# Performance work log

Measured on AMD Instinct MI355X. Metric: run time of the kernel, lower is better.

Reference implementation:

```python
import jax, jax.numpy as jnp
import numpy as np


def xenet_batch(x, a, e, sw, sb, aiw, aib, ajw, ajb, nw, nb, ew, eb):
    """Spektral XENetConvBatch: x (B,N,F), a (B,N,N), e (B,N,N,S)."""
    B, N, F = x.shape
    x_i = jnp.broadcast_to(x[:, :, None, :], (B, N, N, F))   # target node i per pair
    x_j = jnp.broadcast_to(x[:, None, :, :], (B, N, N, F))   # source node j per pair
    e_t = jnp.transpose(e, (0, 2, 1, 3))                      # reversed edge features
    stack = jnp.concatenate([x_i, x_j, e, e_t], axis=-1)      # (B,N,N,2F+2S)
    stack = jax.nn.relu(stack @ sw + sb)                      # stack MLP, (B,N,N,32)
    stack = stack * a[..., None]                              # mask/weight by adjacency
    att_i = jax.nn.sigmoid(stack @ aiw + aib)                 # incoming gate
    att_j = jax.nn.sigmoid(stack @ ajw + ajb)                 # outgoing gate
    agg_i = jnp.sum(att_i * stack, axis=2)                    # aggregate over sources j -> (B,N,32)
    agg_j = jnp.sum(att_j * stack, axis=1)                    # aggregate over targets i -> (B,N,32)
    x_out = jnp.concatenate([x, agg_i, agg_j], axis=-1) @ nw + nb  # node model (linear)
    e_out = stack @ ew + eb                                   # edge model (linear)
    return x_out, e_out


def setup_inputs() -> dict:
    key = jax.random.key(0)
    ks = jax.random.split(key, 16)
    B, N, F, S, C, L = 1, 400, 240, 1, 32, 1440
    SIN = 2 * F + 2 * S   # 482
    NIN = F + 2 * C       # 304
    s = 0.05
    inp = {
        "x": jax.random.normal(ks[0], (B, N, F), jnp.float32),
        "a": jax.random.uniform(ks[1], (B, N, N), jnp.float32),
        "e": jax.random.normal(ks[2], (B, N, N, S), jnp.float32),
        "c1_sw": jax.random.normal(ks[3], (SIN, C), jnp.float32) * s,
        "c1_sb": jnp.zeros((C,), jnp.float32),
        "c1_aiw": jax.random.normal(ks[4], (C, 1), jnp.float32) * s,
        "c1_aib": jnp.zeros((1,), jnp.float32),
        "c1_ajw": jax.random.normal(ks[5], (C, 1), jnp.float32) * s,
        "c1_ajb": jnp.zeros((1,), jnp.float32),
        "c1_nw": jax.random.normal(ks[6], (NIN, F), jnp.float32) * s,
        "c1_nb": jnp.zeros((F,), jnp.float32),
        "c1_ew": jax.random.normal(ks[7], (C, S), jnp.float32) * s,
        "c1_eb": jnp.zeros((S,), jnp.float32),
        "c2_sw": jax.random.normal(ks[8], (SIN, C), jnp.float32) * s,
        "c2_sb": jnp.zeros((C,), jnp.float32),
        "c2_aiw": jax.random.normal(ks[9], (C, 1), jnp.float32) * s,
        "c2_aib": jnp.zeros((1,), jnp.float32),
        "c2_ajw": jax.random.normal(ks[10], (C, 1), jnp.float32) * s,
        "c2_ajb": jnp.zeros((1,), jnp.float32),
        "c2_nw": jax.random.normal(ks[11], (NIN, F), jnp.float32) * s,
        "c2_nb": jnp.zeros((F,), jnp.float32),
        "c2_ew": jax.random.normal(ks[12], (C, S), jnp.float32) * s,
        "c2_eb": jnp.zeros((S,), jnp.float32),
        "dw": jax.random.normal(ks[13], (F, L), jnp.float32) * s,
        "db": jnp.zeros((L,), jnp.float32),
    }
    return inp


def reference(x, a, e,
              c1_sw, c1_sb, c1_aiw, c1_aib, c1_ajw, c1_ajb, c1_nw, c1_nb, c1_ew, c1_eb,
              c2_sw, c2_sb, c2_aiw, c2_aib, c2_ajw, c2_ajb, c2_nw, c2_nb, c2_ew, c2_eb,
              dw, db):
    x, e = xenet_batch(x, a, e, c1_sw, c1_sb, c1_aiw, c1_aib, c1_ajw, c1_ajb,
                       c1_nw, c1_nb, c1_ew, c1_eb)
    x, e = xenet_batch(x, a, e, c2_sw, c2_sb, c2_aiw, c2_aib, c2_ajw, c2_ajb,
                       c2_nw, c2_nb, c2_ew, c2_eb)
    return x @ dw + db  # (B, N, n_labels)
```

## Files before the change

kernel.cpp:

```cpp
#include <hip/hip_runtime.h>

#define NN 400
#define FF 240
#define CC 32
#define NIN 304
#define LL 1440

__global__ __launch_bounds__(256) void pq_kernel(
    const float* __restrict__ x, const float* __restrict__ sw,
    const float* __restrict__ sb, float* __restrict__ P, float* __restrict__ Q) {
    const int i0  = blockIdx.x * 4;
    const int t   = threadIdx.x;
    const int c   = t & 31;
    const int isQ = (t >> 5) & 1;
    const int g   = t >> 6;
    const float* wb = sw + (isQ ? FF * CC : 0) + c;
    const float bias = (!isQ && g == 0) ? sb[c] : 0.0f;
    float acc0 = bias, acc1 = bias, acc2 = bias, acc3 = bias;
    const float* xr = x + i0 * FF;
    const int f0 = g * 60;
    #pragma unroll 4
    for (int f = f0; f < f0 + 60; ++f) {
        const float w = wb[f * CC];
        acc0 += xr[f] * w;
        acc1 += xr[FF + f] * w;
        acc2 += xr[2 * FF + f] * w;
        acc3 += xr[3 * FF + f] * w;
    }
    __shared__ float red[4][256];
    const int slot = t & 63;
    red[g][slot]       = acc0;
    red[g][64 + slot]  = acc1;
    red[g][128 + slot] = acc2;
    red[g][192 + slot] = acc3;
    __syncthreads();
    {
        const int row = t >> 6, s2 = t & 63;
        const float s = red[0][row * 64 + s2] + red[1][row * 64 + s2]
                      + red[2][row * 64 + s2] + red[3][row * 64 + s2];
        const int i = i0 + row;
        if (s2 >= 32) Q[i * CC + (s2 & 31)] = s;
        else          P[i * CC + s2] = s;
    }
}

template<bool WRITE_E, bool DO_PQ>
__global__ __launch_bounds__(1024) void rcf_node(
    const float* __restrict__ P, const float* __restrict__ Q,
    const float* __restrict__ e, const float* __restrict__ a,
    const float* __restrict__ sw_tail,
    const float* __restrict__ aiw, const float* __restrict__ aib,
    const float* __restrict__ ajw, const float* __restrict__ ajb,
    const float* __restrict__ ew, const float* __restrict__ eb,
    float* __restrict__ e_out,
    const float* __restrict__ xin, const float* __restrict__ nw,
    const float* __restrict__ nb,
    const float* __restrict__ sw2, const float* __restrict__ sb2,
    float* __restrict__ xout, float* __restrict__ Pout, float* __restrict__ Qout) {
    const int bid  = blockIdx.x;
    const int base = (bid & 7) * 50 + (bid >> 3) * 2;
    const int t  = threadIdx.x;
    const int pg = t >> 3, l = t & 7, c0 = l * 4;

    __shared__ float smem[10816];
    float* red  = smem;
    float* vA   = smem + 9216;
    float* vB   = smem + 9520;
    float* xsA  = smem + 9824;
    float* xsB  = smem + 10064;
    float* part = smem + 10304;
    float* redn = smem;
    float* red2 = smem;

    if (t < FF) {
        vA[t] = xin[base * FF + t];
        vB[t] = xin[(base + 1) * FF + t];
    }

    float2 er2[4], ak2[4];
    int kk[4];
    #pragma unroll
    for (int it = 0; it < 4; ++it) {
        const int off = it * 128 + pg;
        kk[it] = (off < NN) ? off : 0;
        er2[it] = *(const float2*)(e + kk[it] * NN + base);
        ak2[it] = *(const float2*)(a + kk[it] * NN + base);
    }

    float w1v[4], w2v[4], wiv[4], wjv[4], wev[4];
    *(float4*)w1v = *(const float4*)(sw_tail + c0);
    *(float4*)w2v = *(const float4*)(sw_tail + CC + c0);
    *(float4*)wiv = *(const float4*)(aiw + c0);
    *(float4*)wjv = *(const float4*)(ajw + c0);
    if (WRITE_E) *(float4*)wev = *(const float4*)(ew + c0);
    const float bi = aib[0], bj = ajb[0];
    const float be = WRITE_E ? eb[0] : 0.0f;

    #pragma unroll
    for (int rp = 0; rp < 2; ++rp) {
        const int b = base + rp;
        float* vcur = rp ? vB : vA;

        float Pb[4], Qb[4];
        *(float4*)Pb = *(const float4*)(P + b * CC + c0);
        *(float4*)Qb = *(const float4*)(Q + b * CC + c0);

        float acc_i[4] = {0, 0, 0, 0}, acc_j[4] = {0, 0, 0, 0};
        #pragma unroll
        for (int it = 0; it < 4; ++it) {
            const int off = it * 128 + pg;
            const bool valid = off < NN;
            const int k = kk[it];
            float Qk[4], Pk[4];
            *(float4*)Qk = *(const float4*)(Q + k * CC + c0);
            *(float4*)Pk = *(const float4*)(P + k * CC + c0);
            const float e_f  = e[b * NN + k];
            const float a_bk = a[b * NN + k];
            const float e_r  = rp ? er2[it].y : er2[it].x;
            const float a_kb = rp ? ak2[it].y : ak2[it].x;
            float sr[4], sc[4];
            #pragma unroll
            for (int q = 0; q < 4; ++q) {
                sr[q] = fmaxf(Pb[q] + Qk[q] + e_f * w1v[q] + e_r * w2v[q], 0.0f) * a_bk;
                sc[q] = fmaxf(Pk[q] + Qb[q] + e_r * w1v[q] + e_f * w2v[q], 0.0f) * a_kb;
            }
            float d_i = sr[0] * wiv[0] + sr[1] * wiv[1] + sr[2] * wiv[2] + sr[3] * wiv[3];
            float d_j = sc[0] * wjv[0] + sc[1] * wjv[1] + sc[2] * wjv[2] + sc[3] * wjv[3];
            float d_e = WRITE_E ? (sr[0] * wev[0] + sr[1] * wev[1] + sr[2] * wev[2] + sr[3] * wev[3]) : 0.0f;
            #pragma unroll
            for (int m = 1; m < 8; m <<= 1) {
                d_i += __shfl_xor(d_i, m);
                d_j += __shfl_xor(d_j, m);
                if (WRITE_E) d_e += __shfl_xor(d_e, m);
            }
            const float gi = valid ? __fdividef(1.0f, 1.0f + __expf(-(d_i + bi))) : 0.0f;
            const float gj = valid ? __fdividef(1.0f, 1.0f + __expf(-(d_j + bj))) : 0.0f;
            #pragma unroll
            for (int q = 0; q < 4; ++q) {
                acc_i[q] += gi * sr[q];
                acc_j[q] += gj * sc[q];
            }
            if (WRITE_E && l == 0 && valid) e_out[b * NN + k] = d_e + be;
        }
        #pragma unroll
        for (int q = 0; q < 4; ++q) {
            red[pg * 36 + c0 + q]          = acc_i[q];
            red[(128 + pg) * 36 + c0 + q]  = acc_j[q];
        }
        __syncthreads();
        if (t < 512) {
            const int c = t & 31, sg = (t >> 5) & 7, which = t >> 8;
            float s = 0.0f;
            #pragma unroll
            for (int g2 = sg * 16; g2 < sg * 16 + 16; ++g2)
                s += red[(which * 128 + g2) * 36 + c];
            part[t] = s;
        }
        __syncthreads();
        if (t < 64) {
            const int which = t >> 5, c = t & 31;
            float s = 0.0f;
            #pragma unroll
            for (int sg = 0; sg < 8; ++sg) s += part[which * 256 + sg * 32 + c];
            vcur[FF + t] = s;
        }
        __syncthreads();
    }

    {
        const int fg = t % 60, h = t / 60;
        if (t < 960) {
            const int f0 = fg * 4;
            float4 aA = make_float4(0.f, 0.f, 0.f, 0.f);
            float4 aB = make_float4(0.f, 0.f, 0.f, 0.f);
            const int k0 = h * 19;
            #pragma unroll
            for (int k = k0; k < k0 + 19; ++k) {
                const float4 w = *(const float4*)(nw + k * FF + f0);
                const float va = vA[k], vb = vB[k];
                aA.x += va * w.x; aA.y += va * w.y; aA.z += va * w.z; aA.w += va * w.w;
                aB.x += vb * w.x; aB.y += vb * w.y; aB.z += vb * w.z; aB.w += vb * w.w;
            }
            *(float4*)(redn + h * 240 + f0)        = aA;
            *(float4*)(redn + 3840 + h * 240 + f0) = aB;
        }
    }
    __syncthreads();
    if (t < FF) {
        float rA = nb[t], rB = nb[t];
        #pragma unroll
        for (int h = 0; h < 16; ++h) {
            rA += redn[h * 240 + t];
            rB += redn[3840 + h * 240 + t];
        }
        xout[base * FF + t]       = rA;
        xout[(base + 1) * FF + t] = rB;
        xsA[t] = rA;
        xsB[t] = rB;
    }
    if (DO_PQ) {
        __syncthreads();
        const int c = t & 31, isQ = (t >> 5) & 1, g = t >> 6;
        const float* wb = sw2 + (isQ ? FF * CC : 0) + c;
        const float bias = (!isQ && g == 0) ? sb2[c] : 0.0f;
        float accA = bias, accB = bias;
        const int f0 = g * 15;
        #pragma unroll
        for (int f = f0; f < f0 + 15; ++f) {
            const float w = wb[f * CC];
            accA += xsA[f] * w;
            accB += xsB[f] * w;
        }
        red2[g * 64 + (t & 63)]        = accA;
        red2[1024 + g * 64 + (t & 63)] = accB;
        __syncthreads();
        if (t < 128) {
            const int row = t >> 6, slot = t & 63;
            float s = 0.0f;
            #pragma unroll
            for (int g2 = 0; g2 < 16; ++g2) s += red2[row * 1024 + g2 * 64 + slot];
            const int bb = base + row;
            if (slot >= 32) Qout[bb * CC + (slot & 31)] = s;
            else            Pout[bb * CC + slot] = s;
        }
    }
}

__global__ __launch_bounds__(1024) void dense_kernel(
    const float* __restrict__ x, const float* __restrict__ dw,
    const float* __restrict__ db, float* __restrict__ out) {
    const int i0 = blockIdx.x * 8;
    const int t  = threadIdx.x;
    const int l  = t & 255;
    const int fs = t >> 8;
    const int gl = blockIdx.y * 256 + l;
    __shared__ float xs[8 * FF];
    __shared__ float red[32 * 256];
    for (int idx = t; idx < 8 * FF; idx += 1024) {
        const int r = idx / FF, f = idx - r * FF;
        xs[r * FF + f] = x[(i0 + r) * FF + f];
    }
    __syncthreads();
    float acc[8] = {0, 0, 0, 0, 0, 0, 0, 0};
    if (gl < LL) {
        const int f0 = fs * 60;
        #pragma unroll 4
        for (int f = f0; f < f0 + 60; ++f) {
            const float w = dw[f * LL + gl];
            #pragma unroll
            for (int r = 0; r < 8; ++r) acc[r] += xs[r * FF + f] * w;
        }
    }
    #pragma unroll
    for (int r = 0; r < 8; ++r) red[(fs * 8 + r) * 256 + l] = acc[r];
    __syncthreads();
    if (gl < LL) {
        const int r2 = t >> 8;
        const float d = db[gl];
        #pragma unroll
        for (int rr = r2; rr < 8; rr += 4) {
            const float s = red[(0 + rr) * 256 + l] + red[(8 + rr) * 256 + l]
                          + red[(16 + rr) * 256 + l] + red[(24 + rr) * 256 + l];
            out[(i0 + rr) * LL + gl] = d + s;
        }
    }
}

extern "C" void kernel_launch(void* const* d_in, const int* in_sizes, int n_in,
                              void* d_out, int out_size, void* d_ws, size_t ws_size,
                              hipStream_t stream) {
    const float* x  = (const float*)d_in[0];
    const float* a  = (const float*)d_in[1];
    const float* e0 = (const float*)d_in[2];

    const float* c1_sw  = (const float*)d_in[3];
    const float* c1_sb  = (const float*)d_in[4];
    const float* c1_aiw = (const float*)d_in[5];
    const float* c1_aib = (const float*)d_in[6];
    const float* c1_ajw = (const float*)d_in[7];
    const float* c1_ajb = (const float*)d_in[8];
    const float* c1_nw  = (const float*)d_in[9];
    const float* c1_nb  = (const float*)d_in[10];
    const float* c1_ew  = (const float*)d_in[11];
    const float* c1_eb  = (const float*)d_in[12];

    const float* c2_sw  = (const float*)d_in[13];
    const float* c2_sb  = (const float*)d_in[14];
    const float* c2_aiw = (const float*)d_in[15];
    const float* c2_aib = (const float*)d_in[16];
    const float* c2_ajw = (const float*)d_in[17];
    const float* c2_ajb = (const float*)d_in[18];
    const float* c2_nw  = (const float*)d_in[19];
    const float* c2_nb  = (const float*)d_in[20];
    const float* dw = (const float*)d_in[23];
    const float* db = (const float*)d_in[24];

    float* ws = (float*)d_ws;
    float* P1 = ws;
    float* Q1 = ws + 12800;
    float* P2 = ws + 25600;
    float* Q2 = ws + 38400;
    float* x1 = ws + 51200;
    float* x2 = ws + 147200;
    float* e1 = ws + 243200;

    float* out = (float*)d_out;

    pq_kernel<<<NN / 4, 256, 0, stream>>>(x, c1_sw, c1_sb, P1, Q1);

    rcf_node<true, true><<<NN / 2, 1024, 0, stream>>>(
        P1, Q1, e0, a, c1_sw + 480 * CC,
        c1_aiw, c1_aib, c1_ajw, c1_ajb, c1_ew, c1_eb, e1,
        x, c1_nw, c1_nb, c2_sw, c2_sb, x1, P2, Q2);

    rcf_node<false, false><<<NN / 2, 1024, 0, stream>>>(
        P2, Q2, e1, a, c2_sw + 480 * CC,
        c2_aiw, c2_aib, c2_ajw, c2_ajb, nullptr, nullptr, nullptr,
        x1, c2_nw, c2_nb, nullptr, nullptr, x2, nullptr, nullptr);

    dense_kernel<<<dim3(NN / 8, 6), 1024, 0, stream>>>(x2, dw, db, out);
}
```

Measured before the change: 51.56 us.

## Batch rcf_node reductions across both rows and stage edge output in LDS

The pq kernel goes back to one node per block with 400 blocks instead of 100, trading weight reuse across four rows for more parallelism. In rcf_node the two row passes now write their partial sums to separate LDS regions and share a single two-stage reduction, which removes two of the three barriers per row. Edge outputs are buffered in LDS and written in one coalesced store instead of scattered per-k writes. The cost is a larger LDS footprint (about 84KB for red plus extra buffers), which may limit occupancy.

```diff
diff --git a/kernel.cpp b/kernel.cpp
--- a/kernel.cpp
+++ b/kernel.cpp
@@ -9,38 +9,24 @@
 __global__ __launch_bounds__(256) void pq_kernel(
     const float* __restrict__ x, const float* __restrict__ sw,
     const float* __restrict__ sb, float* __restrict__ P, float* __restrict__ Q) {
-    const int i0  = blockIdx.x * 4;
+    const int i   = blockIdx.x;
     const int t   = threadIdx.x;
     const int c   = t & 31;
     const int isQ = (t >> 5) & 1;
     const int g   = t >> 6;
     const float* wb = sw + (isQ ? FF * CC : 0) + c;
-    const float bias = (!isQ && g == 0) ? sb[c] : 0.0f;
-    float acc0 = bias, acc1 = bias, acc2 = bias, acc3 = bias;
-    const float* xr = x + i0 * FF;
+    float acc = (!isQ && g == 0) ? sb[c] : 0.0f;
+    const float* xr = x + i * FF;
     const int f0 = g * 60;
     #pragma unroll 4
-    for (int f = f0; f < f0 + 60; ++f) {
-        const float w = wb[f * CC];
-        acc0 += xr[f] * w;
-        acc1 += xr[FF + f] * w;
-        acc2 += xr[2 * FF + f] * w;
-        acc3 += xr[3 * FF + f] * w;
-    }
-    __shared__ float red[4][256];
-    const int slot = t & 63;
-    red[g][slot]       = acc0;
-    red[g][64 + slot]  = acc1;
-    red[g][128 + slot] = acc2;
-    red[g][192 + slot] = acc3;
-    __syncthreads();
-    {
-        const int row = t >> 6, s2 = t & 63;
-        const float s = red[0][row * 64 + s2] + red[1][row * 64 + s2]
-                      + red[2][row * 64 + s2] + red[3][row * 64 + s2];
-        const int i = i0 + row;
-        if (s2 >= 32) Q[i * CC + (s2 & 31)] = s;
-        else          P[i * CC + s2] = s;
+    for (int f = f0; f < f0 + 60; ++f) acc += xr[f] * wb[f * CC];
+    __shared__ float red[4][64];
+    red[g][t & 63] = acc;
+    __syncthreads();
+    if (t < 64) {
+        const float s = red[0][t] + red[1][t] + red[2][t] + red[3][t];
+        if (t >= 32) Q[i * CC + (t & 31)] = s;
+        else         P[i * CC + t] = s;
     }
 }
 
@@ -62,15 +48,12 @@
     const int t  = threadIdx.x;
     const int pg = t >> 3, l = t & 7, c0 = l * 4;
 
-    __shared__ float smem[10816];
-    float* red  = smem;
-    float* vA   = smem + 9216;
-    float* vB   = smem + 9520;
-    float* xsA  = smem + 9824;
-    float* xsB  = smem + 10064;
-    float* part = smem + 10304;
-    float* redn = smem;
-    float* red2 = smem;
+    __shared__ float red[4 * 128 * 36];
+    __shared__ float part[1024];
+    __shared__ float vA[304], vB[304], xsA[240], xsB[240];
+    __shared__ float eout_lds[2 * NN];
+    float* redn = red;
+    float* red2 = red;
 
     if (t < FF) {
         vA[t] = xin[base * FF + t];
@@ -99,7 +82,6 @@
     #pragma unroll
     for (int rp = 0; rp < 2; ++rp) {
         const int b = base + rp;
-        float* vcur = rp ? vB : vA;
 
         float Pb[4], Qb[4];
         *(float4*)Pb = *(const float4*)(P + b * CC + c0);
@@ -140,32 +122,37 @@
                 acc_i[q] += gi * sr[q];
                 acc_j[q] += gj * sc[q];
             }
-            if (WRITE_E && l == 0 && valid) e_out[b * NN + k] = d_e + be;
+            if (WRITE_E && l == 0 && valid) eout_lds[rp * NN + k] = d_e + be;
         }
         #pragma unroll
         for (int q = 0; q < 4; ++q) {
-            red[pg * 36 + c0 + q]          = acc_i[q];
-            red[(128 + pg) * 36 + c0 + q]  = acc_j[q];
-        }
-        __syncthreads();
-        if (t < 512) {
-            const int c = t & 31, sg = (t >> 5) & 7, which = t >> 8;
-            float s = 0.0f;
-            #pragma unroll
-            for (int g2 = sg * 16; g2 < sg * 16 + 16; ++g2)
-                s += red[(which * 128 + g2) * 36 + c];
-            part[t] = s;
-        }
-        __syncthreads();
-        if (t < 64) {
-            const int which = t >> 5, c = t & 31;
-            float s = 0.0f;
-            #pragma unroll
-            for (int sg = 0; sg < 8; ++sg) s += part[which * 256 + sg * 32 + c];
-            vcur[FF + t] = s;
-        }
-        __syncthreads();
-    }
+            red[((rp * 2 + 0) * 128 + pg) * 36 + c0 + q] = acc_i[q];
+            red[((rp * 2 + 1) * 128 + pg) * 36 + c0 + q] = acc_j[q];
+        }
+    }
+    __syncthreads();
+
+    if (WRITE_E && t < 2 * NN) e_out[base * NN + t] = eout_lds[t];
+
+    {
+        const int c = t & 31, sg = (t >> 5) & 7, set = t >> 8;
+        float s = 0.0f;
+        #pragma unroll
+        for (int g2 = sg * 16; g2 < sg * 16 + 16; ++g2)
+            s += red[(set * 128 + g2) * 36 + c];
+        part[t] = s;
+    }
+    __syncthreads();
+
+    if (t < 128) {
+        const int set = t >> 5, c = t & 31;
+        float s = 0.0f;
+        #pragma unroll
+        for (int sg = 0; sg < 8; ++sg) s += part[set * 256 + sg * 32 + c];
+        float* vdst = (set < 2) ? vA : vB;
+        vdst[FF + (set & 1) * CC + c] = s;
+    }
+    __syncthreads();
 
     {
         const int fg = t % 60, h = t / 60;
@@ -306,7 +293,7 @@
 
     float* out = (float*)d_out;
 
-    pq_kernel<<<NN / 4, 256, 0, stream>>>(x, c1_sw, c1_sb, P1, Q1);
+    pq_kernel<<<NN, 256, 0, stream>>>(x, c1_sw, c1_sb, P1, Q1);
 
     rcf_node<true, true><<<NN / 2, 1024, 0, stream>>>(
         P1, Q1, e0, a, c1_sw + 480 * CC,
```

Result: faster. 50.05 us, median of 2 (-2.9%).
